# Performance work log

Measured on AMD Instinct MI355X. Metric: run time of the kernel, lower is better.

The kernel has to match this reference:

```python
import jax, jax.numpy as jnp
import numpy as np

B, S, D = 4, 2048, 2048
D_INNER = max(128, D // 2)  # 1024, torch default d_inner
FO = 2                      # filter_order
K = 3                       # kernel_size
KS = 3                      # short_kernel_size


def setup_inputs() -> dict:
    key = jax.random.key(0)
    ks = jax.random.split(key, 6)
    return {
        "x": jax.random.normal(ks[0], (B, S, D), jnp.float32),
        # depthwise short conv: weight (D, KS), bias (D,)
        "short_w": jax.random.normal(ks[1], (D, KS), jnp.float32) / np.float32(np.sqrt(KS)),
        "short_b": jnp.zeros((D,), jnp.float32),
        # filter MLP proj: Linear(D -> FO*D_INNER)
        "proj_w": jax.random.normal(ks[2], (D, FO * D_INNER), jnp.float32) / np.float32(np.sqrt(D)),
        "proj_b": jnp.zeros((FO * D_INNER,), jnp.float32),
        # filter MLP output: Linear(D_INNER -> K), SHARED across filter orders
        "filt_w": jax.random.normal(ks[3], (D_INNER, K), jnp.float32) / np.float32(np.sqrt(D_INNER)),
        "filt_b": jnp.zeros((K,), jnp.float32),
        # output projection Linear(D -> D)
        "out_w": jax.random.normal(ks[4], (D, D), jnp.float32) / np.float32(np.sqrt(D)),
        "out_b": jnp.zeros((D,), jnp.float32),
    }


def reference(x, short_w, short_b, proj_w, proj_b, filt_w, filt_b, out_w, out_b):
    b, s, d = x.shape
    v = x  # v captured BEFORE short-conv residual, as in the torch code

    # --- causal depthwise short conv (pad k-1 on left, truncate to s) ---
    xp = jnp.pad(x, ((0, 0), (KS - 1, 0), (0, 0)))
    x_short = short_b
    for j in range(KS):  # tiny fixed kernel loop
        x_short = x_short + xp[:, j:j + s, :] * short_w[:, j]
    x = x + x_short

    # --- filter function: Linear -> GELU -> (shared) Linear -> tanh ---
    h = jax.nn.gelu(x @ proj_w + proj_b, approximate=False)         # (b, s, FO*D_INNER)
    h = h.reshape(b, s, FO, D_INNER)
    filt = jnp.tanh(jnp.einsum('bsfi,ik->bsfk', h, filt_w) + filt_b)  # (b, s, FO, K)

    # --- gated depthwise conv: kernel = mean over seq, shared across channels;
    # sum over filter orders commutes with the (linear) conv, so fold it in ---
    w = filt.mean(axis=1).sum(axis=1)                                # (b, K)
    xp2 = jnp.pad(x, ((0, 0), (K - 1, 0), (0, 0)))
    conv = jnp.zeros_like(x)
    for j in range(K):
        conv = conv + xp2[:, j:j + s, :] * w[:, j][:, None, None]

    # --- gate with v, GELU, output projection ---
    y = jax.nn.gelu(conv * v, approximate=False)
    return y @ out_w + out_b
```

## Files before the change

kernel.cpp:

```cpp
#include <hip/hip_runtime.h>
#include <hip/hip_bf16.h>
#include <math.h>

typedef unsigned short u16;
typedef __attribute__((ext_vector_type(4))) unsigned short u16x4;
typedef __attribute__((ext_vector_type(8))) unsigned short u16x8;
typedef __attribute__((ext_vector_type(8))) short s16x8;
typedef __attribute__((ext_vector_type(4))) float f32x4;

#define B_  4
#define S_  2048
#define D_  2048
#define DI_ 1024
#define MROWS (B_ * S_)
#define KDIM  D_
#define NDIM  D_
#define STRIP 16

__device__ __forceinline__ float b2f(u16 u) {
    union { unsigned i; float f; } v; v.i = ((unsigned)u) << 16; return v.f;
}
__device__ __forceinline__ u16 f2b(float f) {
    unsigned u = __float_as_uint(f);
    unsigned r = (u + 0x7FFFu + ((u >> 16) & 1u)) >> 16;
    return (u16)r;
}
__device__ __forceinline__ float gelu_exact(float x) {
    return 0.5f * x * (1.0f + erff(x * 0.70710678118654752f));
}

#define GLOAD_LDS16(gp, lp)                                                    \
    __builtin_amdgcn_global_load_lds(                                          \
        (const __attribute__((address_space(1))) void*)(gp),                   \
        (__attribute__((address_space(3))) void*)(lp), 16, 0, 0)

__global__ void transpose_k(const float* __restrict__ in0, u16* __restrict__ out0,
                            const float* __restrict__ in1, u16* __restrict__ out1,
                            int n) {
    __shared__ float tile[32][33];
    const float* in = (blockIdx.z == 0) ? in0 : in1;
    u16* out = (blockIdx.z == 0) ? out0 : out1;
    int bx = blockIdx.x * 32, by = blockIdx.y * 32;
    int tx = threadIdx.x, ty = threadIdx.y;
    for (int i = 0; i < 32; i += 8)
        tile[ty + i][tx] = in[(size_t)(by + ty + i) * n + bx + tx];
    __syncthreads();
    for (int i = 0; i < 32; i += 8)
        out[(size_t)(bx + ty + i) * n + by + tx] = f2b(tile[tx][ty + i]);
}

__global__ void shortconv_k(const float* __restrict__ x, const float* __restrict__ sw,
                            const float* __restrict__ sb, u16* __restrict__ xs,
                            float* __restrict__ wacc, float* __restrict__ t_g) {
    const int bid = blockIdx.y * 2 + blockIdx.x;
    {
        int z = bid * 256 + threadIdx.x;
        if (z < 12) wacc[z] = 0.0f;
        if (z < MROWS * 6) t_g[z] = 0.0f;
    }
    const int c = blockIdx.x * 1024 + threadIdx.x * 4;
    const int r0 = blockIdx.y * STRIP;
    const int t0 = r0 & (S_ - 1);

    float tap[12];
    #pragma unroll
    for (int q = 0; q < 3; ++q)
        ((f32x4*)tap)[q] = *(const f32x4*)(sw + (size_t)c * 3 + q * 4);
    f32x4 sbv = *(const f32x4*)(sb + c);

    const float* base = x + (size_t)r0 * D_ + c;
    f32x4 m2, m1;
    if (t0 == 0) { m2 = (f32x4)(0.0f); m1 = (f32x4)(0.0f); }
    else { m2 = *(const f32x4*)(base - 2 * D_); m1 = *(const f32x4*)(base - D_); }

    u16* op = xs + (size_t)r0 * D_ + c;
    #pragma unroll
    for (int rr = 0; rr < STRIP; ++rr) {
        f32x4 cur = *(const f32x4*)(base + (size_t)rr * D_);
        u16x4 outv;
        #pragma unroll
        for (int e = 0; e < 4; ++e) {
            float v = cur[e] + sbv[e]
                    + tap[e * 3 + 0] * m2[e]
                    + tap[e * 3 + 1] * m1[e]
                    + tap[e * 3 + 2] * cur[e];
            outv[e] = f2b(v);
        }
        *(u16x4*)(op + (size_t)rr * D_) = outv;
        m2 = m1; m1 = cur;
    }
}

#define STG_A(REG, KOFF) do { const u16* _g = gA + (KOFF);                     \
    GLOAD_LDS16(_g, &As[REG][ldsW0]);                                          \
    GLOAD_LDS16(_g + (size_t)128 * KDIM, &As[REG][ldsW1]); } while (0)
#define STG_B(REG, KOFF) do { const u16* _g = gB + (KOFF);                     \
    GLOAD_LDS16(_g, &Bs[REG][ldsW0]);                                          \
    GLOAD_LDS16(_g + (size_t)128 * KDIM, &Bs[REG][ldsW1]); } while (0)
#define LD_AH(R_) do {                                                         \
    aH[0] = *(const s16x8*)&As[R_][aoffR[4]];                                  \
    aH[1] = *(const s16x8*)&As[R_][aoffR[5]];                                  \
    aH[2] = *(const s16x8*)&As[R_][aoffR[6]];                                  \
    aH[3] = *(const s16x8*)&As[R_][aoffR[7]]; } while (0)
#define LD_ALBC(S_, R_) do {                                                   \
    aL[S_][0] = *(const s16x8*)&As[R_][aoffR[0]];                              \
    aL[S_][1] = *(const s16x8*)&As[R_][aoffR[1]];                              \
    aL[S_][2] = *(const s16x8*)&As[R_][aoffR[2]];                              \
    aL[S_][3] = *(const s16x8*)&As[R_][aoffR[3]];                              \
    bC[S_][0] = *(const s16x8*)&Bs[R_][boffR[0]];                              \
    bC[S_][1] = *(const s16x8*)&Bs[R_][boffR[1]];                              \
    bC[S_][2] = *(const s16x8*)&Bs[R_][boffR[2]];                              \
    bC[S_][3] = *(const s16x8*)&Bs[R_][boffR[3]]; } while (0)
#define MFMA_LO(S_) do { __builtin_amdgcn_s_setprio(1);                        \
    _Pragma("unroll")                                                          \
    for (int i_ = 0; i_ < 4; ++i_) {                                           \
        _Pragma("unroll")                                                      \
        for (int j_ = 0; j_ < 4; ++j_)                                         \
            acc[i_][j_] = __builtin_amdgcn_mfma_f32_16x16x32_bf16(             \
                aL[S_][i_], bC[S_][j_], acc[i_][j_], 0, 0, 0);                 \
    }                                                                          \
    __builtin_amdgcn_s_setprio(0); } while (0)
#define MFMA_HI(S_) do { __builtin_amdgcn_s_setprio(1);                        \
    _Pragma("unroll")                                                          \
    for (int i_ = 0; i_ < 4; ++i_) {                                           \
        _Pragma("unroll")                                                      \
        for (int j_ = 0; j_ < 4; ++j_)                                         \
            acc[4 + i_][j_] = __builtin_amdgcn_mfma_f32_16x16x32_bf16(         \
                aH[i_], bC[S_][j_], acc[4 + i_][j_], 0, 0, 0);                 \
    }                                                                          \
    __builtin_amdgcn_s_setprio(0); } while (0)
#define BARR() __builtin_amdgcn_s_barrier()
#define VM8() asm volatile("s_waitcnt vmcnt(8)" ::: "memory")
#define VM4() asm volatile("s_waitcnt vmcnt(4)" ::: "memory")
#define VM0() asm volatile("s_waitcnt vmcnt(0)" ::: "memory")
#define VMNOP()

#define TILE(T_, R_, RN_, CS_, NS_, DOSTG_, GATE_, DOPF_) do {                 \
    BARR();                                                                    \
    if (DOSTG_) { STG_A((((R_) + 3) & 3), ((T_) + 3) * 32);                    \
                  STG_B((((R_) + 3) & 3), ((T_) + 3) * 32); }                  \
    LD_AH(R_);                                                                 \
    MFMA_LO(CS_);                                                              \
    GATE_;                                                                     \
    BARR();                                                                    \
    if (DOPF_) { LD_ALBC(NS_, RN_); }                                          \
    MFMA_HI(CS_);                                                              \
} while (0)

#define GEMM_CORE_OL(APTR, BPTR)                                               \
    __shared__ u16 As[4][8192];                                                \
    __shared__ u16 Bs[4][8192];                                                \
    const int tid  = threadIdx.x;                                              \
    const int wid  = tid >> 6;                                                 \
    const int lane = tid & 63;                                                 \
    const int wr   = wid >> 2;                                                 \
    const int wc   = wid & 3;                                                  \
    const int row0 = blockIdx.y << 8;                                          \
    const int col0 = blockIdx.x << 8;                                          \
    const int rowS    = tid >> 2;                                              \
    const int colOffS = (((tid & 3) ^ ((rowS >> 1) & 3)) << 3);                \
    const u16* gA = (APTR) + (size_t)(row0 + rowS) * KDIM + colOffS;           \
    const u16* gB = (BPTR) + (size_t)(col0 + rowS) * KDIM + colOffS;           \
    const int ldsW0 = wid * 512;                                               \
    const int ldsW1 = 4096 + wid * 512;                                        \
    int aoffR[8], boffR[4];                                                    \
    _Pragma("unroll")                                                          \
    for (int i = 0; i < 8; ++i) {                                              \
        int row  = (wr << 7) + (i << 4) + (lane & 15);                         \
        int slot = (lane >> 4) ^ ((row >> 1) & 3);                             \
        aoffR[i] = row * 32 + slot * 8;                                        \
    }                                                                          \
    _Pragma("unroll")                                                          \
    for (int j = 0; j < 4; ++j) {                                              \
        int row  = (wc << 6) + (j << 4) + (lane & 15);                         \
        int slot = (lane >> 4) ^ ((row >> 1) & 3);                             \
        boffR[j] = row * 32 + slot * 8;                                        \
    }                                                                          \
    f32x4 acc[8][4];                                                           \
    _Pragma("unroll")                                                          \
    for (int i = 0; i < 8; ++i)                                                \
        _Pragma("unroll")                                                      \
        for (int j = 0; j < 4; ++j) acc[i][j] = (f32x4)(0.0f);                 \
    s16x8 aL[2][4], bC[2][4], aH[4];                                           \
    STG_A(0, 0);  STG_B(0, 0);                                                 \
    STG_A(1, 32); STG_B(1, 32);                                                \
    STG_A(2, 64); STG_B(2, 64);                                                \
    VM8();                          \
    BARR();                                                                    \
    LD_ALBC(0, 0);                                       \
    _Pragma("unroll 1")                                                        \
    for (int t = 0; t < 15; ++t) {                                             \
        const int T4 = t * 4;                                                  \
        TILE(T4 + 0, 0, 1, 0, 1, 1, VM8(), 1);                                 \
        TILE(T4 + 1, 1, 2, 1, 0, 1, VM8(), 1);                                 \
        TILE(T4 + 2, 2, 3, 0, 1, 1, VM8(), 1);                                 \
        TILE(T4 + 3, 3, 0, 1, 0, 1, VM8(), 1);                                 \
    }                                                                          \
    TILE(60, 0, 1, 0, 1, 1, VM8(), 1);                                         \
    TILE(61, 1, 2, 1, 0, 0, VM4(), 1);                                         \
    TILE(62, 2, 3, 0, 1, 0, VM0(), 1);                                         \
    TILE(63, 3, 0, 1, 0, 0, VMNOP(), 0);

__global__ __launch_bounds__(512, 2)
void gemm_f8(const u16* __restrict__ A, const u16* __restrict__ BT,
             const float* __restrict__ bias,
             const float* __restrict__ fw, float* __restrict__ t_g) {
    GEMM_CORE_OL(A, BT)

    __shared__ float t_lds[768];
    __syncthreads();
    for (int z = tid; z < 768; z += 512) t_lds[z] = 0.0f;
    __syncthreads();

    const int colt0 = (wc << 6) + (lane & 15);
    float fwv[4][3], bsv[4];
    const int ibase = (col0 & (DI_ - 1)) + colt0;
    #pragma unroll
    for (int j = 0; j < 4; ++j) {
        int ifilt = ibase + j * 16;
        fwv[j][0] = fw[ifilt * 3 + 0];
        fwv[j][1] = fw[ifilt * 3 + 1];
        fwv[j][2] = fw[ifilt * 3 + 2];
        bsv[j] = bias[col0 + colt0 + j * 16];
    }
    #pragma unroll
    for (int i = 0; i < 8; ++i) {
        #pragma unroll
        for (int r = 0; r < 4; ++r) {
            float s0 = 0.f, s1 = 0.f, s2 = 0.f;
            #pragma unroll
            for (int j = 0; j < 4; ++j) {
                float hv = gelu_exact(acc[i][j][r] + bsv[j]);
                s0 += hv * fwv[j][0];
                s1 += hv * fwv[j][1];
                s2 += hv * fwv[j][2];
            }
            #pragma unroll
            for (int m = 1; m < 16; m <<= 1) {
                s0 += __shfl_xor(s0, m, 16);
                s1 += __shfl_xor(s1, m, 16);
                s2 += __shfl_xor(s2, m, 16);
            }
            if ((lane & 15) == 0) {
                int trow = (wr << 7) + ((lane >> 4) << 2) + (i << 4) + r;
                atomicAdd(&t_lds[trow * 3 + 0], s0);
                atomicAdd(&t_lds[trow * 3 + 1], s1);
                atomicAdd(&t_lds[trow * 3 + 2], s2);
            }
        }
    }
    __syncthreads();
    const int f3 = (col0 >= DI_) ? 3 : 0;
    for (int z = tid; z < 768; z += 512) {
        int rr = z / 3, k = z - rr * 3;
        atomicAdd(&t_g[(size_t)(row0 + rr) * 6 + f3 + k], t_lds[z]);
    }
}

__global__ __launch_bounds__(512, 2)
void gemm8_k(const u16* __restrict__ A, const u16* __restrict__ BT,
             const float* __restrict__ bias, float* __restrict__ C) {
    GEMM_CORE_OL(A, BT)

    const int colt0 = (wc << 6) + (lane & 15);
    const int crow0 = row0 + (wr << 7) + ((lane >> 4) << 2);
    #pragma unroll
    for (int j = 0; j < 4; ++j) {
        int col = col0 + colt0 + j * 16;
        float bs = bias[col];
        #pragma unroll
        for (int i = 0; i < 8; ++i) {
            int rbase = crow0 + i * 16;
            #pragma unroll
            for (int r = 0; r < 4; ++r)
                C[(size_t)(rbase + r) * NDIM + col] = acc[i][j][r] + bs;
        }
    }
}

__global__ void filt_finish_k(const float* __restrict__ t_g, const float* __restrict__ fb,
                              float* __restrict__ wacc) {
    __shared__ float part[3];
    const int tid = threadIdx.x;
    if (tid < 3) part[tid] = 0.0f;
    __syncthreads();
    int p = blockIdx.x * 256 + tid;
    int row = p >> 1, f = p & 1;
    const float* tp = t_g + (size_t)row * 6 + f * 3;
    atomicAdd(&part[0], tanhf(tp[0] + fb[0]));
    atomicAdd(&part[1], tanhf(tp[1] + fb[1]));
    atomicAdd(&part[2], tanhf(tp[2] + fb[2]));
    __syncthreads();
    if (tid < 3) {
        int b = blockIdx.x >> 4;
        atomicAdd(&wacc[b * 3 + tid], part[tid]);
    }
}

__global__ void gate_k(const u16* __restrict__ xs, const float* __restrict__ v,
                       const float* __restrict__ wacc, u16* __restrict__ g) {
    const int c = blockIdx.x * 1024 + threadIdx.x * 4;
    const int r0 = blockIdx.y * STRIP;
    const int t0 = r0 & (S_ - 1);
    const int b = r0 >> 11;
    const float w0 = wacc[b * 3 + 0] * (1.0f / (float)S_);
    const float w1 = wacc[b * 3 + 1] * (1.0f / (float)S_);
    const float w2 = wacc[b * 3 + 2] * (1.0f / (float)S_);

    const u16* base = xs + (size_t)r0 * D_ + c;
    f32x4 m2, m1;
    if (t0 == 0) {
        m2 = (f32x4)(0.0f); m1 = (f32x4)(0.0f);
    } else {
        u16x4 a2 = *(const u16x4*)(base - 2 * D_);
        u16x4 a1 = *(const u16x4*)(base - D_);
        #pragma unroll
        for (int e = 0; e < 4; ++e) { m2[e] = b2f(a2[e]); m1[e] = b2f(a1[e]); }
    }

    const float* vp = v + (size_t)r0 * D_ + c;
    u16* op = g + (size_t)r0 * D_ + c;
    #pragma unroll
    for (int rr = 0; rr < STRIP; ++rr) {
        u16x4 cb = *(const u16x4*)(base + (size_t)rr * D_);
        f32x4 vv = *(const f32x4*)(vp + (size_t)rr * D_);
        f32x4 cur;
        #pragma unroll
        for (int e = 0; e < 4; ++e) cur[e] = b2f(cb[e]);
        u16x4 outv;
        #pragma unroll
        for (int e = 0; e < 4; ++e) {
            float conv = w0 * m2[e] + w1 * m1[e] + w2 * cur[e];
            outv[e] = f2b(gelu_exact(conv * vv[e]));
        }
        *(u16x4*)(op + (size_t)rr * D_) = outv;
        m2 = m1; m1 = cur;
    }
}

extern "C" void kernel_launch(void* const* d_in, const int* in_sizes, int n_in,
                              void* d_out, int out_size, void* d_ws, size_t ws_size,
                              hipStream_t stream) {
    const float* x       = (const float*)d_in[0];
    const float* short_w = (const float*)d_in[1];
    const float* short_b = (const float*)d_in[2];
    const float* proj_w  = (const float*)d_in[3];
    const float* proj_b  = (const float*)d_in[4];
    const float* filt_w  = (const float*)d_in[5];
    const float* filt_b  = (const float*)d_in[6];
    const float* out_w   = (const float*)d_in[7];
    const float* out_b   = (const float*)d_in[8];
    float* out = (float*)d_out;

    char* ws = (char*)d_ws;
    const size_t xs_bytes = (size_t)MROWS * D_ * 2;
    const size_t wt_bytes = (size_t)KDIM * NDIM * 2;
    float* wacc = (float*)(ws);
    float* t_g  = (float*)(ws + 1024);
    u16*   xs   = (u16*)(ws + 262144);
    u16*   g    = (u16*)(ws + 262144 + xs_bytes);
    u16*   wT1  = (u16*)(ws + 262144 + 2 * xs_bytes);
    const size_t need_dual = 262144 + 2 * xs_bytes + 2 * wt_bytes;
    const bool dual = (ws_size >= need_dual);
    u16* wT2 = dual ? (u16*)(ws + 262144 + 2 * xs_bytes + wt_bytes) : wT1;

    dim3 tb(32, 8, 1);

    if (dual) {
        dim3 tg(D_ / 32, D_ / 32, 2);
        transpose_k<<<tg, tb, 0, stream>>>(proj_w, wT1, out_w, wT2, D_);
    } else {
        dim3 tg(D_ / 32, D_ / 32, 1);
        transpose_k<<<tg, tb, 0, stream>>>(proj_w, wT1, proj_w, wT1, D_);
    }

    dim3 cg(2, MROWS / STRIP, 1);
    shortconv_k<<<cg, 256, 0, stream>>>(x, short_w, short_b, xs, wacc, t_g);

    dim3 gg(NDIM / 256, MROWS / 256, 1);
    gemm_f8<<<gg, 512, 0, stream>>>(xs, wT1, proj_b, filt_w, t_g);

    filt_finish_k<<<64, 256, 0, stream>>>(t_g, filt_b, wacc);

    if (!dual) {
        dim3 tg(D_ / 32, D_ / 32, 1);
        transpose_k<<<tg, tb, 0, stream>>>(out_w, wT2, out_w, wT2, D_);
    }

    gate_k<<<cg, 256, 0, stream>>>(xs, x, wacc, g);

    gemm8_k<<<gg, 512, 0, stream>>>(g, wT2, out_b, out);
}
```

Measured before the change: 360.2 us.

## Swizzle GEMM block order, add smaller-tile output GEMM, warp-reduce filter sums

New measurement: 354.6 us. No clear change (-1.6%).

```diff
diff --git a/kernel.cpp b/kernel.cpp
--- a/kernel.cpp
+++ b/kernel.cpp
@@ -155,8 +155,10 @@
     const int lane = tid & 63;                                                 \
     const int wr   = wid >> 2;                                                 \
     const int wc   = wid & 3;                                                  \
-    const int row0 = blockIdx.y << 8;                                          \
-    const int col0 = blockIdx.x << 8;                                          \
+    const int lid_ = (blockIdx.y << 3) | blockIdx.x;                           \
+    const int wsw_ = ((lid_ & 7) << 5) | (lid_ >> 3);         \
+    const int row0 = (wsw_ >> 3) << 8;                                         \
+    const int col0 = (wsw_ & 7) << 8;                                          \
     const int rowS    = tid >> 2;                                              \
     const int colOffS = (((tid & 3) ^ ((rowS >> 1) & 3)) << 3);                \
     const u16* gA = (APTR) + (size_t)(row0 + rowS) * KDIM + colOffS;           \
@@ -185,9 +187,9 @@
     STG_A(0, 0);  STG_B(0, 0);                                                 \
     STG_A(1, 32); STG_B(1, 32);                                                \
     STG_A(2, 64); STG_B(2, 64);                                                \
-    VM8();                          \
+    VM8();                                                                     \
     BARR();                                                                    \
-    LD_ALBC(0, 0);                                       \
+    LD_ALBC(0, 0);                                                             \
     _Pragma("unroll 1")                                                        \
     for (int t = 0; t < 15; ++t) {                                             \
         const int T4 = t * 4;                                                  \
@@ -257,10 +259,84 @@
     }
 }
 
-__global__ __launch_bounds__(512, 2)
-void gemm8_k(const u16* __restrict__ A, const u16* __restrict__ BT,
-             const float* __restrict__ bias, float* __restrict__ C) {
-    GEMM_CORE_OL(A, BT)
+__global__ __launch_bounds__(256, 2)
+void gemm2_tlp(const u16* __restrict__ A, const u16* __restrict__ BT,
+               const float* __restrict__ bias, float* __restrict__ C) {
+    __shared__ u16 As[2][8192];
+    __shared__ u16 Bs[2][4096];
+
+    const int tid  = threadIdx.x;
+    const int wid  = tid >> 6;
+    const int lane = tid & 63;
+    const int wr   = wid >> 1;
+    const int wc   = wid & 1;
+    const int lid  = (blockIdx.y << 4) | blockIdx.x;
+    const int wsw  = ((lid & 7) << 6) | (lid >> 3);
+    const int row0 = (wsw >> 4) << 8;
+    const int col0 = (wsw & 15) << 7;
+
+    const int srow = tid >> 2;
+    const int cSw  = (((tid & 3) ^ ((srow >> 1) & 3)) << 3);
+    const u16* gA0 = A  + (size_t)(row0 + srow) * KDIM + cSw;
+    const u16* gB0 = BT + (size_t)(col0 + srow) * KDIM + cSw;
+    const int ldsW = wid * 512;
+
+#define STG2(R_, KOFF) do {                                                    \
+    const u16* _ga = gA0 + (KOFF);                                             \
+    const u16* _gb = gB0 + (KOFF);                                             \
+    GLOAD_LDS16(_ga,                     &As[R_][ldsW]);                       \
+    GLOAD_LDS16(_ga + (size_t)64 * KDIM, &As[R_][2048 + ldsW]);                \
+    GLOAD_LDS16(_ga + (size_t)128 * KDIM, &As[R_][4096 + ldsW]);               \
+    GLOAD_LDS16(_ga + (size_t)192 * KDIM, &As[R_][6144 + ldsW]);               \
+    GLOAD_LDS16(_gb,                     &Bs[R_][ldsW]);                       \
+    GLOAD_LDS16(_gb + (size_t)64 * KDIM, &Bs[R_][2048 + ldsW]);                \
+} while (0)
+
+    int aoffR[8], boffR[4];
+    #pragma unroll
+    for (int i = 0; i < 8; ++i) {
+        int row  = (wr << 7) + (i << 4) + (lane & 15);
+        int slot = (lane >> 4) ^ ((row >> 1) & 3);
+        aoffR[i] = row * 32 + slot * 8;
+    }
+    #pragma unroll
+    for (int j = 0; j < 4; ++j) {
+        int row  = (wc << 6) + (j << 4) + (lane & 15);
+        int slot = (lane >> 4) ^ ((row >> 1) & 3);
+        boffR[j] = row * 32 + slot * 8;
+    }
+
+    f32x4 acc[8][4];
+    #pragma unroll
+    for (int i = 0; i < 8; ++i)
+        #pragma unroll
+        for (int j = 0; j < 4; ++j) acc[i][j] = (f32x4)(0.0f);
+
+    STG2(0, 0);
+    VM0();
+    BARR();
+
+    #pragma unroll 1
+    for (int T = 0; T < 64; ++T) {
+        const int cur = T & 1;
+        if (T < 63) STG2(cur ^ 1, (T + 1) * 32);
+        s16x8 af[8], bf[4];
+        #pragma unroll
+        for (int i = 0; i < 8; ++i) af[i] = *(const s16x8*)&As[cur][aoffR[i]];
+        #pragma unroll
+        for (int j = 0; j < 4; ++j) bf[j] = *(const s16x8*)&Bs[cur][boffR[j]];
+        __builtin_amdgcn_s_setprio(1);
+        #pragma unroll
+        for (int i = 0; i < 8; ++i)
+            #pragma unroll
+            for (int j = 0; j < 4; ++j)
+                acc[i][j] = __builtin_amdgcn_mfma_f32_16x16x32_bf16(
+                    af[i], bf[j], acc[i][j], 0, 0, 0);
+        __builtin_amdgcn_s_setprio(0);
+        VM0();
+        BARR();
+    }
+#undef STG2
 
     const int colt0 = (wc << 6) + (lane & 15);
     const int crow0 = row0 + (wr << 7) + ((lane >> 4) << 2);
@@ -280,20 +356,27 @@
 
 __global__ void filt_finish_k(const float* __restrict__ t_g, const float* __restrict__ fb,
                               float* __restrict__ wacc) {
-    __shared__ float part[3];
+    __shared__ float part[4][3];
     const int tid = threadIdx.x;
-    if (tid < 3) part[tid] = 0.0f;
-    __syncthreads();
     int p = blockIdx.x * 256 + tid;
     int row = p >> 1, f = p & 1;
     const float* tp = t_g + (size_t)row * 6 + f * 3;
-    atomicAdd(&part[0], tanhf(tp[0] + fb[0]));
-    atomicAdd(&part[1], tanhf(tp[1] + fb[1]));
-    atomicAdd(&part[2], tanhf(tp[2] + fb[2]));
+    float v0 = tanhf(tp[0] + fb[0]);
+    float v1 = tanhf(tp[1] + fb[1]);
+    float v2 = tanhf(tp[2] + fb[2]);
+    #pragma unroll
+    for (int m = 1; m < 64; m <<= 1) {
+        v0 += __shfl_xor(v0, m, 64);
+        v1 += __shfl_xor(v1, m, 64);
+        v2 += __shfl_xor(v2, m, 64);
+    }
+    const int wid = tid >> 6, lane = tid & 63;
+    if (lane == 0) { part[wid][0] = v0; part[wid][1] = v1; part[wid][2] = v2; }
     __syncthreads();
     if (tid < 3) {
+        float s = part[0][tid] + part[1][tid] + part[2][tid] + part[3][tid];
         int b = blockIdx.x >> 4;
-        atomicAdd(&wacc[b * 3 + tid], part[tid]);
+        atomicAdd(&wacc[b * 3 + tid], s);
     }
 }
 
@@ -389,5 +472,6 @@
 
     gate_k<<<cg, 256, 0, stream>>>(xs, x, wacc, g);
 
-    gemm8_k<<<gg, 512, 0, stream>>>(g, wT2, out_b, out);
-}
+    dim3 g2(NDIM / 128, MROWS / 256, 1);
+    gemm2_tlp<<<g2, 256, 0, stream>>>(g, wT2, out_b, out);
+}
```
